# Kernel tuning notes

Hardware: AMD Instinct MI355X
Metric: run time of the kernel (lower is better)

The kernel has to match this reference:

```python
import jax, jax.numpy as jnp
import numpy as np

NEURONS = (3072, 8192, 8192, 10)
TSTEPS = 20
THRES = 1.0
DECAY = (2 ** 4 - 1) / 2 ** 4  # 0.9375


def setup_inputs() -> dict:
    key = jax.random.key(0)
    k_img, k1, k2, k3 = jax.random.split(key, 4)
    image = jax.random.uniform(k_img, (NEURONS[0],), dtype=jnp.float32)
    # He-style init matching torch.randn(neu_in, neu_out) * sqrt(2/neu_in)
    W1 = jax.random.normal(k1, (NEURONS[0], NEURONS[1]), dtype=jnp.float32) * np.sqrt(2 / NEURONS[0])
    W2 = jax.random.normal(k2, (NEURONS[1], NEURONS[2]), dtype=jnp.float32) * np.sqrt(2 / NEURONS[1])
    W3 = jax.random.normal(k3, (NEURONS[2], NEURONS[3]), dtype=jnp.float32) * np.sqrt(2 / NEURONS[2])
    return {"image": image, "W1": W1, "W2": W2, "W3": W3}


def _lif(m, spikes_in, W):
    # integrate: mempot += W.T @ spikes_in
    v = m + spikes_in @ W
    fire = (v >= THRES).astype(v.dtype)
    v = v - THRES * fire
    # leaky decay only where the neuron did not fire
    m_new = v * (fire + (1.0 - fire) * DECAY)
    return m_new, fire


def reference(image, W1, W2, W3):
    f32 = jnp.float32
    init = (
        jnp.zeros(NEURONS[0], f32),  # input membrane
        jnp.zeros(NEURONS[1], f32),  # lin1 membrane
        jnp.zeros(NEURONS[2], f32),  # lin2 membrane
        jnp.zeros(NEURONS[3], f32),  # lin3 membrane
        jnp.zeros(NEURONS[1], f32),  # lin1 spikes from previous step (spikes[t])
        jnp.zeros(NEURONS[2], f32),  # lin2 spikes from previous step
    )

    def step(state, _):
        mi, m1, m2, m3, s1_prev, s2_prev = state
        # input layer: integrate-and-fire, no decay
        mi = mi + image
        s_in = (mi >= THRES).astype(f32)
        mi = mi - THRES * s_in
        # lin1 sees input spikes of the SAME step; lin2/lin3 see previous-step
        # spikes of their pre-layer (pipeline delay in original loop)
        m1, s1 = _lif(m1, s_in, W1)
        m2, s2 = _lif(m2, s1_prev, W2)
        m3, s3 = _lif(m3, s2_prev, W3)
        return (mi, m1, m2, m3, s1, s2), s3

    _, s3_seq = jax.lax.scan(step, init, None, length=TSTEPS)
    # original stores lin3 spikes at indices 1..TSTEPS; index 0 stays zero
    spikes_out = jnp.concatenate([jnp.zeros((1, NEURONS[3]), f32), s3_seq], axis=0)
    return spikes_out
```

## Files before the change

kernel.cpp:

```cpp
#include <hip/hip_runtime.h>

#define TSTEPS 20
#define THRESV 1.0f
#define DECAYV 0.9375f

typedef float f32x2 __attribute__((ext_vector_type(2)));

__device__ unsigned g_mask1[3072];
__device__ float g_part1[32][20][8192];
__device__ float g_sum1[TSTEPS][8192];
__device__ unsigned g_mask2[8192];
__device__ float g_part2[64][19][8192];
__device__ float g_sum2[TSTEPS][8192];
__device__ float g_sum3[TSTEPS][16];


__global__ void __launch_bounds__(512)
snn_input_kernel(const float* __restrict__ image) {
    int i = blockIdx.x * 512 + threadIdx.x;
    if (i < 3072) {
        float img = image[i];
        float mi = 0.f;
        unsigned mask = 0;
        #pragma unroll
        for (int t = 0; t < TSTEPS; ++t) {
            mi += img;
            bool fire = (mi >= THRESV);
            if (fire) mi -= THRESV;
            mask |= (unsigned)fire << t;
        }
        g_mask1[i] = mask;
    }
}

struct __align__(16) SMem {
    unsigned short list[8192];
    float partials[512];
    unsigned long long bw[128];
    unsigned pc[128];
    int cntp;
};

template <int NW>
__device__ __forceinline__ int compact_par(const unsigned long long* bits, SMem& sm) {
    int tid = threadIdx.x;
    if (tid < NW) {
        unsigned long long w = bits[tid];
        sm.bw[tid] = w;
        sm.pc[tid] = (unsigned)__popcll(w);
    }
    __syncthreads();
    constexpr int WPW = NW / 8;
    int wave = tid >> 6, lane = tid & 63;
    int w0 = wave * WPW;
    int base = 0;
    for (int i = lane; i < w0; i += 64) base += (int)sm.pc[i];
    #pragma unroll
    for (int off = 1; off < 64; off <<= 1) base += __shfl_xor(base, off);
    if (wave == 0) {
        int tot = 0;
        for (int i = lane; i < NW; i += 64) tot += (int)sm.pc[i];
        #pragma unroll
        for (int off = 1; off < 64; off <<= 1) tot += __shfl_xor(tot, off);
        if (lane == 0) sm.cntp = tot;
    }
    for (int i = 0; i < WPW; ++i) {
        unsigned long long w = sm.bw[w0 + i];
        if ((w >> lane) & 1ull) {
            int pos = base + __popcll(w & ((1ull << lane) - 1ull));
            sm.list[pos] = (unsigned short)(((w0 + i) << 6) + lane);
        }
        base += __popcll(w);
    }
    __syncthreads();
    return sm.cntp;
}

#define GLD2(dst, ptr) \
    asm volatile("global_load_dwordx2 %0, %1, off" : "=v"(dst) : "v"(ptr))
#define WAIT8(a0,a1,a2,a3,a4,a5,a6,a7) \
    asm volatile("s_waitcnt vmcnt(0)" \
        : "+v"(a0),"+v"(a1),"+v"(a2),"+v"(a3),"+v"(a4),"+v"(a5),"+v"(a6),"+v"(a7))

__device__ __forceinline__ void accrow20(f32x2 w, unsigned m, float* ax, float* ay) {
    #pragma unroll
    for (int bb = 0; bb < 20; ++bb)
        if (m & (1u << bb)) { ax[bb] += w.x; ay[bb] += w.y; }
}

__global__ void __launch_bounds__(512)
w1_dense_kernel(const float* __restrict__ W1) {
    __shared__ unsigned msk[96];
    int blk = blockIdx.x;
    int cs = blk >> 5;
    int rb = blk & 31;
    int tid = threadIdx.x;
    if (tid < 96) msk[tid] = g_mask1[rb * 96 + tid];
    __syncthreads();
    int j = cs * 1024 + tid * 2;
    const float* Wp = W1 + (size_t)rb * 96 * 8192 + j;
    float ax[20], ay[20];
    #pragma unroll
    for (int b = 0; b < 20; ++b) { ax[b] = 0.f; ay[b] = 0.f; }
    for (int r = 0; r < 96; r += 8) {
        const float* p = Wp + (size_t)r * 8192;
        f32x2 w0, w1, w2, w3, w4, w5, w6, w7;
        GLD2(w0, p);                GLD2(w1, p + 8192);
        GLD2(w2, p + 2 * 8192);     GLD2(w3, p + 3 * 8192);
        GLD2(w4, p + 4 * 8192);     GLD2(w5, p + 5 * 8192);
        GLD2(w6, p + 6 * 8192);     GLD2(w7, p + 7 * 8192);
        WAIT8(w0, w1, w2, w3, w4, w5, w6, w7);
        accrow20(w0, __builtin_amdgcn_readfirstlane(msk[r    ]), ax, ay);
        accrow20(w1, __builtin_amdgcn_readfirstlane(msk[r + 1]), ax, ay);
        accrow20(w2, __builtin_amdgcn_readfirstlane(msk[r + 2]), ax, ay);
        accrow20(w3, __builtin_amdgcn_readfirstlane(msk[r + 3]), ax, ay);
        accrow20(w4, __builtin_amdgcn_readfirstlane(msk[r + 4]), ax, ay);
        accrow20(w5, __builtin_amdgcn_readfirstlane(msk[r + 5]), ax, ay);
        accrow20(w6, __builtin_amdgcn_readfirstlane(msk[r + 6]), ax, ay);
        accrow20(w7, __builtin_amdgcn_readfirstlane(msk[r + 7]), ax, ay);
    }
    #pragma unroll
    for (int b = 0; b < 20; ++b)
        *(f32x2*)&g_part1[rb][b][j] = (f32x2){ax[b], ay[b]};
}

__global__ void __launch_bounds__(512)
w1_reduce_kernel() {
    int b = blockIdx.x;
    int t = b / 16;
    int j = (b % 16) * 512 + threadIdx.x;
    float s = 0.f;
    #pragma unroll 8
    for (int rb = 0; rb < 32; ++rb)
        s += g_part1[rb][t][j];
    g_sum1[t][j] = s;
}

__global__ void __launch_bounds__(512)
lif1_kernel() {
    int j = blockIdx.x * 512 + threadIdx.x;
    float m = 0.f;
    unsigned mask = 0;
    #pragma unroll
    for (int t = 0; t < TSTEPS; ++t) {
        float v = m + g_sum1[t][j];
        bool fire = (v >= THRESV);
        if (fire) v -= THRESV;
        m = fire ? v : v * DECAYV;
        mask |= (unsigned)fire << t;
    }
    g_mask2[j] = mask;
}

__device__ __forceinline__ void accrow19(f32x2 w, unsigned m, float* ax, float* ay) {
    #pragma unroll
    for (int bb = 0; bb < 19; ++bb)
        if (m & (1u << bb)) { ax[bb] += w.x; ay[bb] += w.y; }
}

__global__ void __launch_bounds__(512)
w2_dense_kernel(const float* __restrict__ W2) {
    __shared__ unsigned msk[128];
    int blk = blockIdx.x;
    int cs = blk >> 6;
    int rb = blk & 63;
    int tid = threadIdx.x;
    if (tid < 128) msk[tid] = g_mask2[rb * 128 + tid];
    __syncthreads();
    int j = cs * 1024 + tid * 2;
    const float* Wp = W2 + (size_t)rb * 128 * 8192 + j;
    float ax[19], ay[19];
    #pragma unroll
    for (int b = 0; b < 19; ++b) { ax[b] = 0.f; ay[b] = 0.f; }
    for (int r = 0; r < 128; r += 8) {
        const float* p = Wp + (size_t)r * 8192;
        f32x2 w0, w1, w2, w3, w4, w5, w6, w7;
        GLD2(w0, p);                GLD2(w1, p + 8192);
        GLD2(w2, p + 2 * 8192);     GLD2(w3, p + 3 * 8192);
        GLD2(w4, p + 4 * 8192);     GLD2(w5, p + 5 * 8192);
        GLD2(w6, p + 6 * 8192);     GLD2(w7, p + 7 * 8192);
        WAIT8(w0, w1, w2, w3, w4, w5, w6, w7);
        accrow19(w0, __builtin_amdgcn_readfirstlane(msk[r    ]), ax, ay);
        accrow19(w1, __builtin_amdgcn_readfirstlane(msk[r + 1]), ax, ay);
        accrow19(w2, __builtin_amdgcn_readfirstlane(msk[r + 2]), ax, ay);
        accrow19(w3, __builtin_amdgcn_readfirstlane(msk[r + 3]), ax, ay);
        accrow19(w4, __builtin_amdgcn_readfirstlane(msk[r + 4]), ax, ay);
        accrow19(w5, __builtin_amdgcn_readfirstlane(msk[r + 5]), ax, ay);
        accrow19(w6, __builtin_amdgcn_readfirstlane(msk[r + 6]), ax, ay);
        accrow19(w7, __builtin_amdgcn_readfirstlane(msk[r + 7]), ax, ay);
    }
    #pragma unroll
    for (int b = 0; b < 19; ++b)
        *(f32x2*)&g_part2[rb][b][j] = (f32x2){ax[b], ay[b]};
}

__global__ void __launch_bounds__(512)
w2_reduce_kernel() {
    int b = blockIdx.x;
    int t = 1 + b / 16;
    int j = (b % 16) * 512 + threadIdx.x;
    float s = 0.f;
    #pragma unroll 8
    for (int rb = 0; rb < 64; ++rb)
        s += g_part2[rb][t - 1][j];
    g_sum2[t][j] = s;
}

__global__ void __launch_bounds__(512)
lif2_kernel(unsigned long long* __restrict__ s2_bits) {
    int j = blockIdx.x * 512 + threadIdx.x;
    int lane = threadIdx.x & 63;
    float m = 0.f;
    for (int t = 1; t < TSTEPS; ++t) {
        float v = m + g_sum2[t][j];
        bool fire = (v >= THRESV);
        if (fire) v -= THRESV;
        m = fire ? v : v * DECAYV;
        unsigned long long bm = __ballot(fire);
        if (lane == 0) s2_bits[(size_t)t * 128 + (j >> 6)] = bm;
    }
}

__global__ void __launch_bounds__(512)
w3_sums_kernel(const float* __restrict__ W3,
               const unsigned long long* __restrict__ s2_bits) {
    __shared__ SMem sm;
    int t = blockIdx.x + 1;
    int tid = threadIdx.x;
    int count = compact_par<128>(s2_bits + (size_t)(t - 1) * 128, sm);
    int col = tid & 15, g = tid >> 4;
    float acc = 0.f;
    if (col < 10) {
        for (int k = g; k < count; k += 32)
            acc += W3[(size_t)sm.list[k] * 10 + col];
    }
    sm.partials[g * 16 + col] = acc;
    __syncthreads();
    if (tid < 10) {
        float s = 0.f;
        for (int gg = 0; gg < 32; ++gg) s += sm.partials[gg * 16 + tid];
        g_sum3[t][tid] = s;
    }
}

__global__ void w3_lif_kernel(float* __restrict__ out) {
    int tid = threadIdx.x;
    if (tid < 10) {
        float m = 0.f;
        for (int t = 1; t < TSTEPS; ++t) {
            float v = m + g_sum3[t][tid];
            bool fire = (v >= THRESV);
            if (fire) v -= THRESV;
            m = fire ? v : v * DECAYV;
            out[(t + 1) * 10 + tid] = fire ? 1.f : 0.f;
        }
    }
}

extern "C" void kernel_launch(void* const* d_in, const int* in_sizes, int n_in,
                              void* d_out, int out_size, void* d_ws, size_t ws_size,
                              hipStream_t stream) {
    const float* image = (const float*)d_in[0];
    const float* W1 = (const float*)d_in[1];
    const float* W2 = (const float*)d_in[2];
    const float* W3 = (const float*)d_in[3];
    float* out = (float*)d_out;

    unsigned long long* s2_bits = (unsigned long long*)d_ws;

    hipMemsetAsync(d_ws, 0, 20480, stream);
    hipMemsetAsync(d_out, 0, (size_t)out_size * sizeof(float), stream);

    snn_input_kernel<<<6, 512, 0, stream>>>(image);
    w1_dense_kernel<<<8 * 32, 512, 0, stream>>>(W1);
    w1_reduce_kernel<<<20 * 16, 512, 0, stream>>>();
    lif1_kernel<<<16, 512, 0, stream>>>();
    w2_dense_kernel<<<8 * 64, 512, 0, stream>>>(W2);
    w2_reduce_kernel<<<19 * 16, 512, 0, stream>>>();
    lif2_kernel<<<16, 512, 0, stream>>>(s2_bits);
    w3_sums_kernel<<<TSTEPS - 1, 512, 0, stream>>>(W3, s2_bits);
    w3_lif_kernel<<<1, 64, 0, stream>>>(out);
}
```

Baseline: 164.0 us.

## Fuse input spike generation into W1 kernel, drop memsets, widen W2 loads

The input-layer integrate-and-fire loop now runs inside the W1 dense kernel, so the separate input kernel and its global mask buffer are gone. The two workspace and output memsets are removed: lif2_kernel zeroes the t=0 spike words and w3_lif_kernel zeroes output rows 0 and 1. The W2 dense kernel now loads dwordx4 per thread with f32x4 accumulators over half as many blocks. The aim is fewer launches and API calls plus wider memory transactions, at the cost of more accumulator registers and fewer blocks in the W2 pass.

Measured after the change: 294.9 us. 79.9% more time.

```diff
diff --git a/kernel.cpp b/kernel.cpp
--- a/kernel.cpp
+++ b/kernel.cpp
@@ -5,8 +5,8 @@
 #define DECAYV 0.9375f
 
 typedef float f32x2 __attribute__((ext_vector_type(2)));
-
-__device__ unsigned g_mask1[3072];
+typedef float f32x4 __attribute__((ext_vector_type(4)));
+
 __device__ float g_part1[32][20][8192];
 __device__ float g_sum1[TSTEPS][8192];
 __device__ unsigned g_mask2[8192];
@@ -15,11 +15,72 @@
 __device__ float g_sum3[TSTEPS][16];
 
 
-__global__ void __launch_bounds__(512)
-snn_input_kernel(const float* __restrict__ image) {
-    int i = blockIdx.x * 512 + threadIdx.x;
-    if (i < 3072) {
-        float img = image[i];
+struct __align__(16) SMem {
+    unsigned short list[8192];
+    float partials[512];
+    unsigned long long bw[128];
+    unsigned pc[128];
+    int cntp;
+};
+
+template <int NW>
+__device__ __forceinline__ int compact_par(const unsigned long long* bits, SMem& sm) {
+    int tid = threadIdx.x;
+    if (tid < NW) {
+        unsigned long long w = bits[tid];
+        sm.bw[tid] = w;
+        sm.pc[tid] = (unsigned)__popcll(w);
+    }
+    __syncthreads();
+    constexpr int WPW = NW / 8;
+    int wave = tid >> 6, lane = tid & 63;
+    int w0 = wave * WPW;
+    int base = 0;
+    for (int i = lane; i < w0; i += 64) base += (int)sm.pc[i];
+    #pragma unroll
+    for (int off = 1; off < 64; off <<= 1) base += __shfl_xor(base, off);
+    if (wave == 0) {
+        int tot = 0;
+        for (int i = lane; i < NW; i += 64) tot += (int)sm.pc[i];
+        #pragma unroll
+        for (int off = 1; off < 64; off <<= 1) tot += __shfl_xor(tot, off);
+        if (lane == 0) sm.cntp = tot;
+    }
+    for (int i = 0; i < WPW; ++i) {
+        unsigned long long w = sm.bw[w0 + i];
+        if ((w >> lane) & 1ull) {
+            int pos = base + __popcll(w & ((1ull << lane) - 1ull));
+            sm.list[pos] = (unsigned short)(((w0 + i) << 6) + lane);
+        }
+        base += __popcll(w);
+    }
+    __syncthreads();
+    return sm.cntp;
+}
+
+#define GLD2(dst, ptr) \
+    asm volatile("global_load_dwordx2 %0, %1, off" : "=v"(dst) : "v"(ptr))
+#define GLD4(dst, ptr) \
+    asm volatile("global_load_dwordx4 %0, %1, off" : "=v"(dst) : "v"(ptr))
+#define WAIT8(a0,a1,a2,a3,a4,a5,a6,a7) \
+    asm volatile("s_waitcnt vmcnt(0)" \
+        : "+v"(a0),"+v"(a1),"+v"(a2),"+v"(a3),"+v"(a4),"+v"(a5),"+v"(a6),"+v"(a7))
+
+__device__ __forceinline__ void accrow20(f32x2 w, unsigned m, float* ax, float* ay) {
+    #pragma unroll
+    for (int bb = 0; bb < 20; ++bb)
+        if (m & (1u << bb)) { ax[bb] += w.x; ay[bb] += w.y; }
+}
+
+__global__ void __launch_bounds__(512)
+w1_dense_kernel(const float* __restrict__ W1, const float* __restrict__ image) {
+    __shared__ unsigned msk[96];
+    int blk = blockIdx.x;
+    int cs = blk >> 5;
+    int rb = blk & 31;
+    int tid = threadIdx.x;
+    if (tid < 96) {
+        float img = image[rb * 96 + tid];
         float mi = 0.f;
         unsigned mask = 0;
         #pragma unroll
@@ -29,73 +90,8 @@
             if (fire) mi -= THRESV;
             mask |= (unsigned)fire << t;
         }
-        g_mask1[i] = mask;
-    }
-}
-
-struct __align__(16) SMem {
-    unsigned short list[8192];
-    float partials[512];
-    unsigned long long bw[128];
-    unsigned pc[128];
-    int cntp;
-};
-
-template <int NW>
-__device__ __forceinline__ int compact_par(const unsigned long long* bits, SMem& sm) {
-    int tid = threadIdx.x;
-    if (tid < NW) {
-        unsigned long long w = bits[tid];
-        sm.bw[tid] = w;
-        sm.pc[tid] = (unsigned)__popcll(w);
-    }
-    __syncthreads();
-    constexpr int WPW = NW / 8;
-    int wave = tid >> 6, lane = tid & 63;
-    int w0 = wave * WPW;
-    int base = 0;
-    for (int i = lane; i < w0; i += 64) base += (int)sm.pc[i];
-    #pragma unroll
-    for (int off = 1; off < 64; off <<= 1) base += __shfl_xor(base, off);
-    if (wave == 0) {
-        int tot = 0;
-        for (int i = lane; i < NW; i += 64) tot += (int)sm.pc[i];
-        #pragma unroll
-        for (int off = 1; off < 64; off <<= 1) tot += __shfl_xor(tot, off);
-        if (lane == 0) sm.cntp = tot;
-    }
-    for (int i = 0; i < WPW; ++i) {
-        unsigned long long w = sm.bw[w0 + i];
-        if ((w >> lane) & 1ull) {
-            int pos = base + __popcll(w & ((1ull << lane) - 1ull));
-            sm.list[pos] = (unsigned short)(((w0 + i) << 6) + lane);
-        }
-        base += __popcll(w);
-    }
-    __syncthreads();
-    return sm.cntp;
-}
-
-#define GLD2(dst, ptr) \
-    asm volatile("global_load_dwordx2 %0, %1, off" : "=v"(dst) : "v"(ptr))
-#define WAIT8(a0,a1,a2,a3,a4,a5,a6,a7) \
-    asm volatile("s_waitcnt vmcnt(0)" \
-        : "+v"(a0),"+v"(a1),"+v"(a2),"+v"(a3),"+v"(a4),"+v"(a5),"+v"(a6),"+v"(a7))
-
-__device__ __forceinline__ void accrow20(f32x2 w, unsigned m, float* ax, float* ay) {
-    #pragma unroll
-    for (int bb = 0; bb < 20; ++bb)
-        if (m & (1u << bb)) { ax[bb] += w.x; ay[bb] += w.y; }
-}
-
-__global__ void __launch_bounds__(512)
-w1_dense_kernel(const float* __restrict__ W1) {
-    __shared__ unsigned msk[96];
-    int blk = blockIdx.x;
-    int cs = blk >> 5;
-    int rb = blk & 31;
-    int tid = threadIdx.x;
-    if (tid < 96) msk[tid] = g_mask1[rb * 96 + tid];
+        msk[tid] = mask;
+    }
     __syncthreads();
     int j = cs * 1024 + tid * 2;
     const float* Wp = W1 + (size_t)rb * 96 * 8192 + j;
@@ -152,10 +148,10 @@
     g_mask2[j] = mask;
 }
 
-__device__ __forceinline__ void accrow19(f32x2 w, unsigned m, float* ax, float* ay) {
+__device__ __forceinline__ void accrow19_4(f32x4 w, unsigned m, f32x4* acc) {
     #pragma unroll
     for (int bb = 0; bb < 19; ++bb)
-        if (m & (1u << bb)) { ax[bb] += w.x; ay[bb] += w.y; }
+        if (m & (1u << bb)) acc[bb] += w;
 }
 
 __global__ void __launch_bounds__(512)
@@ -167,31 +163,31 @@
     int tid = threadIdx.x;
     if (tid < 128) msk[tid] = g_mask2[rb * 128 + tid];
     __syncthreads();
-    int j = cs * 1024 + tid * 2;
+    int j = cs * 2048 + tid * 4;
     const float* Wp = W2 + (size_t)rb * 128 * 8192 + j;
-    float ax[19], ay[19];
-    #pragma unroll
-    for (int b = 0; b < 19; ++b) { ax[b] = 0.f; ay[b] = 0.f; }
+    f32x4 acc[19];
+    #pragma unroll
+    for (int b = 0; b < 19; ++b) acc[b] = (f32x4){0.f, 0.f, 0.f, 0.f};
     for (int r = 0; r < 128; r += 8) {
         const float* p = Wp + (size_t)r * 8192;
-        f32x2 w0, w1, w2, w3, w4, w5, w6, w7;
-        GLD2(w0, p);                GLD2(w1, p + 8192);
-        GLD2(w2, p + 2 * 8192);     GLD2(w3, p + 3 * 8192);
-        GLD2(w4, p + 4 * 8192);     GLD2(w5, p + 5 * 8192);
-        GLD2(w6, p + 6 * 8192);     GLD2(w7, p + 7 * 8192);
+        f32x4 w0, w1, w2, w3, w4, w5, w6, w7;
+        GLD4(w0, p);                GLD4(w1, p + 8192);
+        GLD4(w2, p + 2 * 8192);     GLD4(w3, p + 3 * 8192);
+        GLD4(w4, p + 4 * 8192);     GLD4(w5, p + 5 * 8192);
+        GLD4(w6, p + 6 * 8192);     GLD4(w7, p + 7 * 8192);
         WAIT8(w0, w1, w2, w3, w4, w5, w6, w7);
-        accrow19(w0, __builtin_amdgcn_readfirstlane(msk[r    ]), ax, ay);
-        accrow19(w1, __builtin_amdgcn_readfirstlane(msk[r + 1]), ax, ay);
-        accrow19(w2, __builtin_amdgcn_readfirstlane(msk[r + 2]), ax, ay);
-        accrow19(w3, __builtin_amdgcn_readfirstlane(msk[r + 3]), ax, ay);
-        accrow19(w4, __builtin_amdgcn_readfirstlane(msk[r + 4]), ax, ay);
-        accrow19(w5, __builtin_amdgcn_readfirstlane(msk[r + 5]), ax, ay);
-        accrow19(w6, __builtin_amdgcn_readfirstlane(msk[r + 6]), ax, ay);
-        accrow19(w7, __builtin_amdgcn_readfirstlane(msk[r + 7]), ax, ay);
+        accrow19_4(w0, __builtin_amdgcn_readfirstlane(msk[r    ]), acc);
+        accrow19_4(w1, __builtin_amdgcn_readfirstlane(msk[r + 1]), acc);
+        accrow19_4(w2, __builtin_amdgcn_readfirstlane(msk[r + 2]), acc);
+        accrow19_4(w3, __builtin_amdgcn_readfirstlane(msk[r + 3]), acc);
+        accrow19_4(w4, __builtin_amdgcn_readfirstlane(msk[r + 4]), acc);
+        accrow19_4(w5, __builtin_amdgcn_readfirstlane(msk[r + 5]), acc);
+        accrow19_4(w6, __builtin_amdgcn_readfirstlane(msk[r + 6]), acc);
+        accrow19_4(w7, __builtin_amdgcn_readfirstlane(msk[r + 7]), acc);
     }
     #pragma unroll
     for (int b = 0; b < 19; ++b)
-        *(f32x2*)&g_part2[rb][b][j] = (f32x2){ax[b], ay[b]};
+        *(f32x4*)&g_part2[rb][b][j] = acc[b];
 }
 
 __global__ void __launch_bounds__(512)
@@ -210,6 +206,7 @@
 lif2_kernel(unsigned long long* __restrict__ s2_bits) {
     int j = blockIdx.x * 512 + threadIdx.x;
     int lane = threadIdx.x & 63;
+    if (lane == 0) s2_bits[j >> 6] = 0ull;
     float m = 0.f;
     for (int t = 1; t < TSTEPS; ++t) {
         float v = m + g_sum2[t][j];
@@ -246,6 +243,8 @@
 __global__ void w3_lif_kernel(float* __restrict__ out) {
     int tid = threadIdx.x;
     if (tid < 10) {
+        out[tid] = 0.f;
+        out[10 + tid] = 0.f;
         float m = 0.f;
         for (int t = 1; t < TSTEPS; ++t) {
             float v = m + g_sum3[t][tid];
@@ -268,14 +267,10 @@
 
     unsigned long long* s2_bits = (unsigned long long*)d_ws;
 
-    hipMemsetAsync(d_ws, 0, 20480, stream);
-    hipMemsetAsync(d_out, 0, (size_t)out_size * sizeof(float), stream);
-
-    snn_input_kernel<<<6, 512, 0, stream>>>(image);
-    w1_dense_kernel<<<8 * 32, 512, 0, stream>>>(W1);
+    w1_dense_kernel<<<8 * 32, 512, 0, stream>>>(W1, image);
     w1_reduce_kernel<<<20 * 16, 512, 0, stream>>>();
     lif1_kernel<<<16, 512, 0, stream>>>();
-    w2_dense_kernel<<<8 * 64, 512, 0, stream>>>(W2);
+    w2_dense_kernel<<<4 * 64, 512, 0, stream>>>(W2);
     w2_reduce_kernel<<<19 * 16, 512, 0, stream>>>();
     lif2_kernel<<<16, 512, 0, stream>>>(s2_bits);
     w3_sums_kernel<<<TSTEPS - 1, 512, 0, stream>>>(W3, s2_bits);
```
